# Optimization experiments

Hardware: AMD Instinct MI355X
Metric: run time of the kernel (lower is better)

The kernel has to match this reference:

```python
import jax, jax.numpy as jnp
import numpy as np

NUM_LAYERS = 2
VOCAB = 32000
INPUT = 1024
HIDDEN = 1024
OUTPUT = 32000
BATCH = 8
SEQ = 256


def setup_inputs() -> dict:
    key = jax.random.key(0)
    ks = jax.random.split(key, 8)
    s_in = 1.0 / np.sqrt(INPUT)
    s_h = 1.0 / np.sqrt(HIDDEN)
    input_ = jax.random.randint(ks[0], (BATCH, SEQ), 0, VOCAB)
    emb = jax.random.normal(ks[1], (VOCAB, INPUT), jnp.float32)
    # Gate order along last dim: [i, f, g, o], each of width HIDDEN.
    Wx = jax.random.uniform(ks[2], (NUM_LAYERS, INPUT, 4 * HIDDEN), jnp.float32, -s_in, s_in)
    bx = jax.random.uniform(ks[3], (NUM_LAYERS, 4 * HIDDEN), jnp.float32, -s_in, s_in)
    Wh = jax.random.uniform(ks[4], (NUM_LAYERS, HIDDEN, 4 * HIDDEN), jnp.float32, -s_h, s_h)
    bh = jax.random.uniform(ks[5], (NUM_LAYERS, 4 * HIDDEN), jnp.float32, -s_h, s_h)
    Wd = jax.random.uniform(ks[6], (HIDDEN, OUTPUT), jnp.float32, -s_h, s_h)
    bd = jax.random.uniform(ks[7], (OUTPUT,), jnp.float32, -s_h, s_h)
    return {"input_": input_, "emb": emb, "Wx": Wx, "bx": bx, "Wh": Wh, "bh": bh, "Wd": Wd, "bd": bd}


def _lstm_core(input_, emb, Wx, bx, Wh, bh, Wd, bd):
    x = emb[input_]                      # [B, T, E]
    xs = jnp.swapaxes(x, 0, 1)           # [T, B, E]
    h0 = jnp.zeros((NUM_LAYERS, x.shape[0], HIDDEN), x.dtype)
    c0 = jnp.zeros_like(h0)

    def step(carry, x_t):
        h, c = carry
        layer_in = x_t
        new_h, new_c = [], []
        for l in range(NUM_LAYERS):
            gates = layer_in @ Wx[l] + bx[l] + h[l] @ Wh[l] + bh[l]  # [B, 4H]
            i_g, f_g, g_g, o_g = jnp.split(gates, 4, axis=-1)
            i_g = jax.nn.sigmoid(i_g)
            f_g = jax.nn.sigmoid(f_g)
            o_g = jax.nn.sigmoid(o_g)
            g_g = jnp.tanh(g_g)
            c_l = f_g * c[l] + i_g * g_g
            h_l = o_g * jnp.tanh(c_l)
            new_h.append(h_l)
            new_c.append(c_l)
            layer_in = h_l
        return (jnp.stack(new_h), jnp.stack(new_c)), layer_in

    (_, _), tops = jax.lax.scan(step, (h0, c0), xs)  # tops: [T, B, H]
    out = tops @ Wd + bd                              # [T, B, V]
    return jnp.swapaxes(out, 0, 1)                    # [B, T, V]


def reference(input_, emb, Wx, bx, Wh, bh, Wd, bd):
    return _lstm_core(input_, emb, Wx, bx, Wh, bh, Wd, bd)
```

## Files before the change

### kernel.cpp

```cpp
#include <hip/hip_runtime.h>
#include <cstdint>
#include <cstddef>

#define BATCH 8
#define SEQ   256
#define HID   1024
#define GATES 4096
#define VOC   32000

typedef __attribute__((ext_vector_type(8))) short bf16x8;
typedef __attribute__((ext_vector_type(4))) float f32x4;

__device__ __forceinline__ float sigf(float x){ return 1.0f/(1.0f + __expf(-x)); }
__device__ __forceinline__ float tanhf_(float x){ return 1.0f - 2.0f/(__expf(2.0f*x) + 1.0f); }

__device__ __forceinline__ unsigned short f2bf(float x){
  union { float f; unsigned u; } v; v.f = x;
  unsigned r = v.u + 0x7fffu + ((v.u >> 16) & 1u);
  return (unsigned short)(r >> 16);
}
__device__ __forceinline__ float bf2f(unsigned short h){
  union { float f; unsigned u; } v; v.u = ((unsigned)h) << 16; return v.f;
}

__global__ void k_init(unsigned* __restrict__ flags, unsigned* __restrict__ hbu){
  int tid = blockIdx.x*blockDim.x + threadIdx.x;
  int nt = gridDim.x*blockDim.x;
  for (int i = tid; i < 256*16; i += nt) flags[i] = 0u;
  for (int i = tid; i < 16384; i += nt) hbu[i] = 0u;
}

template<int AMODE, int OMODE>
__global__ __launch_bounds__(256) void k_mfma(
    const float* __restrict__ A,
    const float* __restrict__ W,
    const float* __restrict__ b1,
    const float* __restrict__ b2,
    const int*   __restrict__ tokens,
    const float* __restrict__ emb,
    float* __restrict__ C, int N)
{
  __shared__ unsigned short AsH[16*1024], AsL[16*1024];
  __shared__ unsigned short BsH[8*1024],  BsL[8*1024];
  int tid = threadIdx.x;
  int m0 = blockIdx.y*256, n0 = blockIdx.x*128;
  int w = tid >> 6, l = tid & 63;
  int lrow = l & 15, kg = l >> 4;

  f32x4 acc[4][8];
  #pragma unroll
  for (int i=0;i<4;i++){
    #pragma unroll
    for (int j=0;j<8;j++) acc[i][j] = (f32x4){0.f,0.f,0.f,0.f};
  }

  int rA  = tid >> 3, fq = tid & 7;

  const float* arow[8];
  #pragma unroll
  for (int i=0;i<8;i++){
    int gm = m0 + rA + 32*i;
    if (AMODE==1) arow[i] = emb + (size_t)tokens[(gm&7)*SEQ + (gm>>3)]*1024;
    else          arow[i] = A   + (size_t)gm*1024;
  }

  for (int kt=0; kt<32; ++kt){
    int k0 = kt*32;
    float4 av[8];
    #pragma unroll
    for (int i=0;i<8;i++)
      av[i] = *(const float4*)(arow[i] + k0 + fq*4);
    float4 wv[4];
    #pragma unroll
    for (int i=0;i<4;i++)
      wv[i] = *(const float4*)(W + (size_t)(k0 + rA)*N + n0 + fq*4 + 32*i);
    __syncthreads();
    #pragma unroll
    for (int i=0;i<8;i++){
      int r = rA + 32*i;
      int base = (r >> 4)*1024 + ((fq >> 1)*16 + (r & 15))*8 + (fq & 1)*4;
      float xs[4] = {av[i].x, av[i].y, av[i].z, av[i].w};
      unsigned long long ph = 0ull, pl = 0ull;
      #pragma unroll
      for (int c=0;c<4;c++){
        unsigned short h = f2bf(xs[c]);
        unsigned short lo = f2bf(xs[c] - bf2f(h));
        ph |= ((unsigned long long)h) << (16*c);
        pl |= ((unsigned long long)lo) << (16*c);
      }
      *(unsigned long long*)&AsH[base] = ph;
      *(unsigned long long*)&AsL[base] = pl;
    }
    #pragma unroll
    for (int i=0;i<4;i++){
      float xs[4] = {wv[i].x, wv[i].y, wv[i].z, wv[i].w};
      #pragma unroll
      for (int c=0;c<4;c++){
        int col = fq*4 + 32*i + c;
        int idx = (col >> 4)*1024 + ((rA >> 3)*16 + (col & 15))*8 + (rA & 7);
        unsigned short h = f2bf(xs[c]);
        BsH[idx] = h;
        BsL[idx] = f2bf(xs[c] - bf2f(h));
      }
    }
    __syncthreads();
    bf16x8 ah[4], al[4];
    #pragma unroll
    for (int i=0;i<4;i++){
      int fi = w*4 + i;
      ah[i] = *(const bf16x8*)&AsH[fi*1024 + l*8];
      al[i] = *(const bf16x8*)&AsL[fi*1024 + l*8];
    }
    #pragma unroll
    for (int jh=0;jh<2;jh++){
      bf16x8 bh_[4], bl_[4];
      #pragma unroll
      for (int j=0;j<4;j++){
        bh_[j] = *(const bf16x8*)&BsH[(jh*4+j)*1024 + l*8];
        bl_[j] = *(const bf16x8*)&BsL[(jh*4+j)*1024 + l*8];
      }
      #pragma unroll
      for (int i=0;i<4;i++){
        #pragma unroll
        for (int j=0;j<4;j++){
          f32x4 a = acc[i][jh*4+j];
          a = __builtin_amdgcn_mfma_f32_16x16x32_bf16(ah[i], bh_[j], a, 0,0,0);
          a = __builtin_amdgcn_mfma_f32_16x16x32_bf16(ah[i], bl_[j], a, 0,0,0);
          a = __builtin_amdgcn_mfma_f32_16x16x32_bf16(al[i], bh_[j], a, 0,0,0);
          acc[i][jh*4+j] = a;
        }
      }
    }
    __syncthreads();
  }

  int mbase = m0 + w*64 + kg*4;
  #pragma unroll
  for (int jj=0;jj<8;jj++){
    int gn = n0 + jj*16 + lrow;
    float bias = b1[gn];
    if (b2) bias += b2[gn];
    #pragma unroll
    for (int i=0;i<4;i++){
      #pragma unroll
      for (int r=0;r<4;r++){
        int m = mbase + i*16 + r;
        size_t crow = (OMODE==1) ? (size_t)((m & 7)*SEQ + (m >> 3)) : (size_t)m;
        C[crow*(size_t)N + gn] = acc[i][jj][r] + bias;
      }
    }
  }
}

__global__ __launch_bounds__(256) void k_rec2(
    const float* __restrict__ G,
    const float* __restrict__ Wh,
    const float* __restrict__ Wx,
    const float* __restrict__ bx1,
    const float* __restrict__ bh1,
    float* __restrict__ Tops,
    unsigned* __restrict__ hbu,
    unsigned* __restrict__ flags)
{
  extern __shared__ char ldsb[];
  unsigned short* A0 = (unsigned short*)ldsb;
  unsigned short* A1 = A0 + 16384;
  unsigned short* A2 = A1 + 16384;
  unsigned short* hB = A2 + 16384;
  float* Cx = (float*)(ldsb + 131072);
  int tid = threadIdx.x;
  int u0 = blockIdx.x*4;
  const int wv = tid >> 6, ln = tid & 63;
  const int fs0 = tid*16, fs1 = (tid+64)*16, fs2 = (tid+128)*16, fs3 = (tid+192)*16;

  {
    int m = tid >> 4, kseg = tid & 15;
    int col = (m >> 2)*1024 + u0 + (m & 3);
    const float* wsrc[3] = { Wh, Wx + (size_t)HID*GATES, Wh + (size_t)HID*GATES };
    unsigned short* Ad[3] = { A0, A1, A2 };
    for (int tgt=0; tgt<3; ++tgt){
      const float* s = wsrc[tgt] + col;
      #pragma unroll
      for (int run=0; run<8; ++run){
        int k0 = kseg*64 + run*8;
        int kt = k0 >> 5, kg = (k0 >> 3) & 3;
        bf16x8 v;
        #pragma unroll
        for (int e=0;e<8;e++) v[e] = (short)f2bf(s[(size_t)(k0+e)*GATES]);
        *(bf16x8*)&Ad[tgt][kt*512 + ((kg<<4)|m)*8] = v;
      }
    }
  }
  float b1r[4] = {0.f,0.f,0.f,0.f};
  if (tid >= 32 && tid < 64){
    int j = tid & 3;
    #pragma unroll
    for (int g=0;g<4;g++) b1r[g] = bx1[g*1024+u0+j] + bh1[g*1024+u0+j];
  }
  float creg = 0.0f;

  for (int p=0; p<=SEQ; ++p){
    const unsigned* h0b = hbu + (size_t)(p&1)*4096;
    const unsigned* h1b = hbu + 8192 + (size_t)((p+1)&1)*4096;
    {
      int colp = tid & 15, seg0 = tid >> 4;
      #pragma unroll
      for (int i=0;i<2;i++){
        int seg = seg0 + 16*i;
        const float* src = (const float*)(((colp < 8) ? h0b : h1b)
                                          + (colp & 7)*512 + seg*16);
        float4 r0,r1,r2,r3;
        asm volatile(
          "global_load_dwordx4 %0, %4, off sc0 sc1\n\t"
          "global_load_dwordx4 %1, %4, off offset:16 sc0 sc1\n\t"
          "global_load_dwordx4 %2, %4, off offset:32 sc0 sc1\n\t"
          "global_load_dwordx4 %3, %4, off offset:48 sc0 sc1\n\t"
          "s_waitcnt vmcnt(0)"
          : "=&v"(r0),"=&v"(r1),"=&v"(r2),"=&v"(r3)
          : "v"(src)
          : "memory");
        *(float4*)&hB[seg*512 + ((0<<4)|colp)*8] = r0;
        *(float4*)&hB[seg*512 + ((1<<4)|colp)*8] = r1;
        *(float4*)&hB[seg*512 + ((2<<4)|colp)*8] = r2;
        *(float4*)&hB[seg*512 + ((3<<4)|colp)*8] = r3;
      }
    }
    float gp0=0.f,gp1=0.f,gp2=0.f,gp3=0.f;
    if (tid < 32 && p < SEQ){
      const float* gp = G + ((size_t)p*8 + (tid>>2))*GATES + u0 + (tid&3);
      gp0 = gp[0]; gp1 = gp[1024]; gp2 = gp[2048]; gp3 = gp[3072];
    }
    __syncthreads();

    f32x4 C0 = {0.f,0.f,0.f,0.f}, C1 = {0.f,0.f,0.f,0.f}, C2 = {0.f,0.f,0.f,0.f};
    #pragma unroll
    for (int kti=0; kti<8; ++kti){
      int kt = wv + kti*4;
      bf16x8 bB = *(const bf16x8*)&hB[kt*512 + ln*8];
      bf16x8 a0 = *(const bf16x8*)&A0[kt*512 + ln*8];
      bf16x8 a1 = *(const bf16x8*)&A1[kt*512 + ln*8];
      bf16x8 a2 = *(const bf16x8*)&A2[kt*512 + ln*8];
      C0 = __builtin_amdgcn_mfma_f32_16x16x32_bf16(a0, bB, C0, 0,0,0);
      C1 = __builtin_amdgcn_mfma_f32_16x16x32_bf16(a1, bB, C1, 0,0,0);
      C2 = __builtin_amdgcn_mfma_f32_16x16x32_bf16(a2, bB, C2, 0,0,0);
    }
    {
      int cn = ln & 15, mb = (ln >> 4)*4;
      #pragma unroll
      for (int r=0;r<4;r++){
        Cx[((wv*3+0)*16 + mb+r)*17 + cn] = C0[r];
        Cx[((wv*3+1)*16 + mb+r)*17 + cn] = C1[r];
        Cx[((wv*3+2)*16 + mb+r)*17 + cn] = C2[r];
      }
    }
    __syncthreads();

    float hv = 0.f; bool pub = false; unsigned dstbase = 0;
    if (tid < 32){
      if (p < SEQ){
        int b = tid >> 2, j = tid & 3;
        float gv0=gp0, gv1=gp1, gv2=gp2, gv3=gp3;
        #pragma unroll
        for (int w=0;w<4;w++){
          gv0 += Cx[((w*3+0)*16 + 0*4+j)*17 + b];
          gv1 += Cx[((w*3+0)*16 + 1*4+j)*17 + b];
          gv2 += Cx[((w*3+0)*16 + 2*4+j)*17 + b];
          gv3 += Cx[((w*3+0)*16 + 3*4+j)*17 + b];
        }
        float iv = sigf(gv0), fv = sigf(gv1), ov = sigf(gv3), gg = tanhf_(gv2);
        creg = fv*creg + iv*gg;
        hv = ov * tanhf_(creg);
        pub = true; dstbase = ((unsigned)(p+1)&1u)*4096u;
      }
    } else if (tid < 64){
      if (p > 0){
        int b = (tid-32) >> 2, j = tid & 3;
        float gv0=b1r[0], gv1=b1r[1], gv2=b1r[2], gv3=b1r[3];
        #pragma unroll
        for (int w=0;w<4;w++){
          gv0 += Cx[((w*3+1)*16 + 0*4+j)*17 + b] + Cx[((w*3+2)*16 + 0*4+j)*17 + b+8];
          gv1 += Cx[((w*3+1)*16 + 1*4+j)*17 + b] + Cx[((w*3+2)*16 + 1*4+j)*17 + b+8];
          gv2 += Cx[((w*3+1)*16 + 2*4+j)*17 + b] + Cx[((w*3+2)*16 + 2*4+j)*17 + b+8];
          gv3 += Cx[((w*3+1)*16 + 3*4+j)*17 + b] + Cx[((w*3+2)*16 + 3*4+j)*17 + b+8];
        }
        float iv = sigf(gv0), fv = sigf(gv1), ov = sigf(gv3), gg = tanhf_(gv2);
        creg = fv*creg + iv*gg;
        hv = ov * tanhf_(creg);
        pub = true; dstbase = 8192u + ((unsigned)p&1u)*4096u;
        Tops[((size_t)(p-1)*8 + b)*HID + u0 + (tid&3)] = hv;
      }
    }
    if (tid < 64){
      unsigned mybits = (unsigned)f2bf(hv);
      unsigned other  = (unsigned)__shfl_xor((int)mybits, 1);
      if (pub && ((tid & 1) == 0)){
        unsigned word = (mybits & 0xffffu) | (other << 16);
        int b = (tid & 31) >> 2;
        int widx = (u0 >> 1) + ((tid >> 1) & 1);
        (void)__hip_atomic_exchange(&hbu[dstbase + b*512 + widx], word,
                                    __ATOMIC_RELAXED, __HIP_MEMORY_SCOPE_AGENT);
      }
    }

    if (p < SEQ){
      if (tid < 64){
        if (tid == 0){
          asm volatile("s_waitcnt vmcnt(0)" ::: "memory");
          (void)__hip_atomic_exchange(&flags[blockIdx.x*16], (unsigned)(p+1),
                                      __ATOMIC_RELAXED, __HIP_MEMORY_SCOPE_AGENT);
        }
        unsigned tgt = (unsigned)(p+1);
        int spins = 0;
        for (;;){
          unsigned a = __hip_atomic_load(&flags[fs0], __ATOMIC_RELAXED, __HIP_MEMORY_SCOPE_AGENT);
          unsigned b = __hip_atomic_load(&flags[fs1], __ATOMIC_RELAXED, __HIP_MEMORY_SCOPE_AGENT);
          unsigned c = __hip_atomic_load(&flags[fs2], __ATOMIC_RELAXED, __HIP_MEMORY_SCOPE_AGENT);
          unsigned d = __hip_atomic_load(&flags[fs3], __ATOMIC_RELAXED, __HIP_MEMORY_SCOPE_AGENT);
          bool ok = (a >= tgt) && (b >= tgt) && (c >= tgt) && (d >= tgt);
          if (__all(ok)) break;
          __builtin_amdgcn_s_sleep(1);
          if (++spins > 150000){
            for (;;){
              unsigned a2 = __hip_atomic_load(&flags[fs0], __ATOMIC_ACQUIRE, __HIP_MEMORY_SCOPE_AGENT);
              unsigned b2 = __hip_atomic_load(&flags[fs1], __ATOMIC_ACQUIRE, __HIP_MEMORY_SCOPE_AGENT);
              unsigned c2 = __hip_atomic_load(&flags[fs2], __ATOMIC_ACQUIRE, __HIP_MEMORY_SCOPE_AGENT);
              unsigned d2 = __hip_atomic_load(&flags[fs3], __ATOMIC_ACQUIRE, __HIP_MEMORY_SCOPE_AGENT);
              bool ok2 = (a2 >= tgt) && (b2 >= tgt) && (c2 >= tgt) && (d2 >= tgt);
              if (__all(ok2)) break;
              __builtin_amdgcn_s_sleep(8);
              if (++spins > 8000000) break;
            }
            break;
          }
        }
      }
      __syncthreads();
    }
  }
}

extern "C" void kernel_launch(void* const* d_in, const int* in_sizes, int n_in,
                              void* d_out, int out_size, void* d_ws, size_t ws_size,
                              hipStream_t stream) {
  const int*   tokens = (const int*)d_in[0];
  const float* emb = (const float*)d_in[1];
  const float* Wx  = (const float*)d_in[2];
  const float* bx  = (const float*)d_in[3];
  const float* Wh  = (const float*)d_in[4];
  const float* bh  = (const float*)d_in[5];
  const float* Wd  = (const float*)d_in[6];
  const float* bd  = (const float*)d_in[7];
  float* out = (float*)d_out;
  float* ws  = (float*)d_ws;

  float* G    = ws;
  float* Tops = ws + (size_t)8388608;
  unsigned* hbu   = (unsigned*)(ws + (size_t)10485760);
  unsigned* flags = (unsigned*)(ws + (size_t)10502144);

  (void)hipFuncSetAttribute((const void*)k_rec2,
        hipFuncAttributeMaxDynamicSharedMemorySize, 144128);

  k_init<<<32,256,0,stream>>>(flags, hbu);

  k_mfma<1,0><<<dim3(32,8),256,0,stream>>>(nullptr, Wx, bx, bh, tokens, emb, G, GATES);

  k_rec2<<<256,256,144128,stream>>>(G, Wh, Wx, bx + GATES, bh + GATES,
                                    Tops, hbu, flags);

  k_mfma<0,1><<<dim3(250,8),256,0,stream>>>(Tops, Wd, bd, nullptr, nullptr, nullptr, out, VOC);
}
```

Measured before the change: 2.109 ms.

## Pre-split recurrence outputs and Wd into bf16 hi/lo pairs for projection GEMM

The recurrent kernel now writes its top-layer outputs directly as bf16 high/low split arrays instead of fp32, so the projection GEMM no longer converts A tiles per block. When the workspace is large enough, a separate pass converts Wd once per call into bf16 hi/lo arrays, and a new projection kernel loads these pre-split weights. This removes conversion work that was repeated across the 8 row-blocks that each reread Wd. In exchange it adds a full conversion pass over the 128MB Wd and reads the same number of bytes as before (two bf16 halves instead of one fp32).

Result: no change. 2.119 ms (+0.5%).

```diff
diff --git a/kernel.cpp b/kernel.cpp
--- a/kernel.cpp
+++ b/kernel.cpp
@@ -28,6 +28,27 @@
   int nt = gridDim.x*blockDim.x;
   for (int i = tid; i < 256*16; i += nt) flags[i] = 0u;
   for (int i = tid; i < 16384; i += nt) hbu[i] = 0u;
+}
+
+__global__ void k_wconv(const float* __restrict__ W,
+                        unsigned short* __restrict__ WH,
+                        unsigned short* __restrict__ WL){
+  const int total4 = (HID*VOC) >> 2;
+  int stride = gridDim.x*blockDim.x;
+  for (int i = blockIdx.x*blockDim.x + threadIdx.x; i < total4; i += stride){
+    float4 v = *(const float4*)(W + (size_t)i*4);
+    float xs[4] = {v.x, v.y, v.z, v.w};
+    unsigned hh = 0, ll = 0;
+    #pragma unroll
+    for (int c=0;c<4;c++){
+      unsigned short h = f2bf(xs[c]);
+      unsigned short lo = f2bf(xs[c] - bf2f(h));
+      hh |= ((unsigned)h)  << (16*(c&1));
+      ll |= ((unsigned)lo) << (16*(c&1));
+      if (c==1){ ((unsigned*)&WH[(size_t)i*4])[0] = hh; ((unsigned*)&WL[(size_t)i*4])[0] = ll; hh=0; ll=0; }
+      if (c==3){ ((unsigned*)&WH[(size_t)i*4])[1] = hh; ((unsigned*)&WL[(size_t)i*4])[1] = ll; }
+    }
+  }
 }
 
 template<int AMODE, int OMODE>
@@ -152,13 +173,130 @@
   }
 }
 
+template<int WPRE>
+__global__ __launch_bounds__(256) void k_proj(
+    const unsigned short* __restrict__ AH,
+    const unsigned short* __restrict__ AL,
+    const float* __restrict__ Wf,
+    const unsigned short* __restrict__ WH,
+    const unsigned short* __restrict__ WL,
+    const float* __restrict__ bd,
+    float* __restrict__ C)
+{
+  __shared__ unsigned short AsH[16*1024], AsL[16*1024];
+  __shared__ unsigned short BsH[8*1024],  BsL[8*1024];
+  int tid = threadIdx.x;
+  int m0 = blockIdx.y*256, n0 = blockIdx.x*128;
+  int w = tid >> 6, l = tid & 63;
+  int lrow = l & 15, kg = l >> 4;
+
+  f32x4 acc[4][8];
+  #pragma unroll
+  for (int i=0;i<4;i++){
+    #pragma unroll
+    for (int j=0;j<8;j++) acc[i][j] = (f32x4){0.f,0.f,0.f,0.f};
+  }
+
+  int rA = tid >> 3, fq = tid & 7;
+
+  for (int kt=0; kt<32; ++kt){
+    int k0 = kt*32;
+    uint2 avh[8], avl[8];
+    #pragma unroll
+    for (int i=0;i<8;i++){
+      size_t off = (size_t)(m0 + rA + 32*i)*1024 + k0 + fq*4;
+      avh[i] = *(const uint2*)&AH[off];
+      avl[i] = *(const uint2*)&AL[off];
+    }
+    uint2 wvh[4], wvl[4];
+    float4 wvf[4];
+    #pragma unroll
+    for (int i=0;i<4;i++){
+      size_t off = (size_t)(k0 + rA)*VOC + n0 + fq*4 + 32*i;
+      if (WPRE){ wvh[i] = *(const uint2*)&WH[off]; wvl[i] = *(const uint2*)&WL[off]; }
+      else     { wvf[i] = *(const float4*)(Wf + off); }
+    }
+    __syncthreads();
+    #pragma unroll
+    for (int i=0;i<8;i++){
+      int r = rA + 32*i;
+      int base = (r >> 4)*1024 + ((fq >> 1)*16 + (r & 15))*8 + (fq & 1)*4;
+      *(uint2*)&AsH[base] = avh[i];
+      *(uint2*)&AsL[base] = avl[i];
+    }
+    #pragma unroll
+    for (int i=0;i<4;i++){
+      #pragma unroll
+      for (int c=0;c<4;c++){
+        int col = fq*4 + 32*i + c;
+        int idx = (col >> 4)*1024 + ((rA >> 3)*16 + (col & 15))*8 + (rA & 7);
+        if (WPRE){
+          BsH[idx] = ((const unsigned short*)&wvh[i])[c];
+          BsL[idx] = ((const unsigned short*)&wvl[i])[c];
+        } else {
+          float xs = (c==0)?wvf[i].x:(c==1)?wvf[i].y:(c==2)?wvf[i].z:wvf[i].w;
+          unsigned short h = f2bf(xs);
+          BsH[idx] = h;
+          BsL[idx] = f2bf(xs - bf2f(h));
+        }
+      }
+    }
+    __syncthreads();
+    bf16x8 ah[4], al[4];
+    #pragma unroll
+    for (int i=0;i<4;i++){
+      int fi = w*4 + i;
+      ah[i] = *(const bf16x8*)&AsH[fi*1024 + l*8];
+      al[i] = *(const bf16x8*)&AsL[fi*1024 + l*8];
+    }
+    #pragma unroll
+    for (int jh=0;jh<2;jh++){
+      bf16x8 bh_[4], bl_[4];
+      #pragma unroll
+      for (int j=0;j<4;j++){
+        bh_[j] = *(const bf16x8*)&BsH[(jh*4+j)*1024 + l*8];
+        bl_[j] = *(const bf16x8*)&BsL[(jh*4+j)*1024 + l*8];
+      }
+      #pragma unroll
+      for (int i=0;i<4;i++){
+        #pragma unroll
+        for (int j=0;j<4;j++){
+          f32x4 a = acc[i][jh*4+j];
+          a = __builtin_amdgcn_mfma_f32_16x16x32_bf16(ah[i], bh_[j], a, 0,0,0);
+          a = __builtin_amdgcn_mfma_f32_16x16x32_bf16(ah[i], bl_[j], a, 0,0,0);
+          a = __builtin_amdgcn_mfma_f32_16x16x32_bf16(al[i], bh_[j], a, 0,0,0);
+          acc[i][jh*4+j] = a;
+        }
+      }
+    }
+    __syncthreads();
+  }
+
+  int mbase = m0 + w*64 + kg*4;
+  #pragma unroll
+  for (int jj=0;jj<8;jj++){
+    int gn = n0 + jj*16 + lrow;
+    float bias = bd[gn];
+    #pragma unroll
+    for (int i=0;i<4;i++){
+      #pragma unroll
+      for (int r=0;r<4;r++){
+        int m = mbase + i*16 + r;
+        size_t crow = (size_t)((m & 7)*SEQ + (m >> 3));
+        C[crow*(size_t)VOC + gn] = acc[i][jj][r] + bias;
+      }
+    }
+  }
+}
+
 __global__ __launch_bounds__(256) void k_rec2(
     const float* __restrict__ G,
     const float* __restrict__ Wh,
     const float* __restrict__ Wx,
     const float* __restrict__ bx1,
     const float* __restrict__ bh1,
-    float* __restrict__ Tops,
+    unsigned short* __restrict__ TopsH,
+    unsigned short* __restrict__ TopsL,
     unsigned* __restrict__ hbu,
     unsigned* __restrict__ flags)
 {
@@ -287,7 +425,11 @@
         creg = fv*creg + iv*gg;
         hv = ov * tanhf_(creg);
         pub = true; dstbase = 8192u + ((unsigned)p&1u)*4096u;
-        Tops[((size_t)(p-1)*8 + b)*HID + u0 + (tid&3)] = hv;
+        unsigned short hi = f2bf(hv);
+        unsigned short lo = f2bf(hv - bf2f(hi));
+        size_t off = ((size_t)(p-1)*8 + b)*HID + u0 + (tid&3);
+        TopsH[off] = hi;
+        TopsL[off] = lo;
       }
     }
     if (tid < 64){
@@ -353,20 +495,29 @@
   float* out = (float*)d_out;
   float* ws  = (float*)d_ws;
 
-  float* G    = ws;
-  float* Tops = ws + (size_t)8388608;
+  float* G = ws;
+  unsigned short* TopsH = (unsigned short*)(ws + (size_t)8388608);
+  unsigned short* TopsL = (unsigned short*)(ws + (size_t)9437184);
   unsigned* hbu   = (unsigned*)(ws + (size_t)10485760);
   unsigned* flags = (unsigned*)(ws + (size_t)10502144);
+  unsigned short* WdH = (unsigned short*)(ws + (size_t)10506240);
+  unsigned short* WdL = (unsigned short*)(ws + (size_t)26890240);
+  const bool wpre = ws_size >= (size_t)43274240*4;
 
   (void)hipFuncSetAttribute((const void*)k_rec2,
         hipFuncAttributeMaxDynamicSharedMemorySize, 144128);
 
   k_init<<<32,256,0,stream>>>(flags, hbu);
+  if (wpre)
+    k_wconv<<<2048,256,0,stream>>>(Wd, WdH, WdL);
 
   k_mfma<1,0><<<dim3(32,8),256,0,stream>>>(nullptr, Wx, bx, bh, tokens, emb, G, GATES);
 
   k_rec2<<<256,256,144128,stream>>>(G, Wh, Wx, bx + GATES, bh + GATES,
-                                    Tops, hbu, flags);
-
-  k_mfma<0,1><<<dim3(250,8),256,0,stream>>>(Tops, Wd, bd, nullptr, nullptr, nullptr, out, VOC);
-}
+                                    TopsH, TopsL, hbu, flags);
+
+  if (wpre)
+    k_proj<1><<<dim3(250,8),256,0,stream>>>(TopsH, TopsL, nullptr, WdH, WdL, bd, out);
+  else
+    k_proj<0><<<dim3(250,8),256,0,stream>>>(TopsH, TopsL, Wd, nullptr, nullptr, bd, out);
+}
```
